# Optimization experiments

Measured on AMD Instinct MI355X. Metric: run time of the kernel, lower is better.

## Reference

```python
import jax, jax.numpy as jnp
import numpy as np

B, L, D, DI, N, R = 2, 2048, 1024, 2048, 16, 64


def setup_inputs() -> dict:
    key = jax.random.key(0)
    ks = jax.random.split(key, 10)
    g = lambda k, shape, s: (jax.random.normal(k, shape, dtype=jnp.float32) * s)
    return {
        "x": g(ks[0], (B, L, D), 1.0),
        "in_w": g(ks[1], (DI, D), 0.02),
        "in_b": jnp.zeros((DI,), jnp.float32),
        "conv_w": g(ks[2], (DI, 1, 3), 0.2),
        "conv_b": jnp.zeros((DI,), jnp.float32),
        "x_proj_w": g(ks[3], (R + N, DI), 0.02),
        "x_proj_b": jnp.zeros((R + N,), jnp.float32),
        "dt_w": g(ks[4], (DI, R), 0.02),
        "dt_b": jnp.zeros((DI,), jnp.float32),
        "A_log": g(ks[5], (DI, N), 1.0),
        "D_param": g(ks[6], (DI,), 1.0),
        "out_w": g(ks[7], (D, DI), 0.02),
        "out_b": jnp.zeros((D,), jnp.float32),
    }


def _forward(x, in_w, in_b, conv_w, conv_b, x_proj_w, x_proj_b,
             dt_w, dt_b, A_log, D_param, out_w, out_b):
    b, l, d = x.shape
    di = in_w.shape[0]
    # in_proj
    h = x @ in_w.T + in_b                               # [b, l, di]
    # depthwise conv1d, kernel 3, padding 1 (output length == l, so the
    # torch [:, :, :l] slice is a no-op)
    hc = jnp.transpose(h, (0, 2, 1))                    # [b, di, l]
    hc = jax.lax.conv_general_dilated(
        hc, conv_w, window_strides=(1,), padding=[(1, 1)],
        dimension_numbers=("NCH", "OIH", "NCH"), feature_group_count=di)
    hc = hc + conv_b[None, :, None]
    u = jax.nn.silu(jnp.transpose(hc, (0, 2, 1)))       # [b, l, di]
    # ssm (dropout is identity in eval mode)
    A = -jnp.exp(A_log)                                 # [di, n]
    x_dbl = u @ x_proj_w.T + x_proj_b                   # [b, l, r+n]
    r = dt_w.shape[1]
    delta_lr, Bm = x_dbl[..., :r], x_dbl[..., r:]       # [b,l,r], [b,l,n]
    delta = jax.nn.softplus(delta_lr @ dt_w.T + dt_b)   # [b, l, di]
    deltaA = jnp.exp(jnp.einsum("bld,dn->bldn", delta, A))        # [b,l,di,n]
    deltaBu = jnp.einsum("bld,bln->bldn", delta * u, Bm)          # [b,l,di,n]

    def step(carry, inp):
        dA, dBu = inp
        carry = dA * carry + dBu
        return carry, carry.sum(-1)

    init = jnp.zeros((b, di, A.shape[1]), dtype=deltaA.dtype)
    _, ys = jax.lax.scan(step, init,
                         (jnp.swapaxes(deltaA, 0, 1), jnp.swapaxes(deltaBu, 0, 1)))
    y = jnp.swapaxes(ys, 0, 1) + u * D_param            # [b, l, di]
    return y @ out_w.T + out_b                          # [b, l, d]


def reference(x, in_w, in_b, conv_w, conv_b, x_proj_w, x_proj_b,
              dt_w, dt_b, A_log, D_param, out_w, out_b):
    return _forward(x, in_w, in_b, conv_w, conv_b, x_proj_w, x_proj_b,
                    dt_w, dt_b, A_log, D_param, out_w, out_b)
```

## Files before the change

kernel.cpp:

```cpp
#include <hip/hip_runtime.h>

#define B_  2
#define L_  2048
#define D_  1024
#define DI_ 2048
#define NS  16
#define RR  64
#define MM  (B_*L_)
#define NC  32
#define CL  (L_/NC)
#define XKS 8

typedef __attribute__((ext_vector_type(8))) short bf16x8;
typedef __attribute__((ext_vector_type(4))) float f32x4;

__device__ __forceinline__ ushort f2bf_rn(float f) {
    union { float f; unsigned u; } v; v.f = f;
    unsigned r = v.u + 0x7FFF + ((v.u >> 16) & 1);
    return (ushort)(r >> 16);
}
__device__ __forceinline__ float bf2f(ushort h) {
    union { unsigned u; float f; } v; v.u = ((unsigned)h) << 16;
    return v.f;
}
__device__ __forceinline__ void gload_lds16(const ushort* g, ushort* l) {
    __builtin_amdgcn_global_load_lds(
        (const __attribute__((address_space(1))) void*)(g),
        (__attribute__((address_space(3))) void*)(l), 16, 0, 0);
}

__global__ __launch_bounds__(256)
void cvt_hilo(const float* __restrict__ in, ushort* __restrict__ hi,
              ushort* __restrict__ lo, int n4)
{
    int i = blockIdx.x * 256 + threadIdx.x;
    if (i >= n4) return;
    float4 v = ((const float4*)in)[i];
    ushort4 h, l;
    h.x = f2bf_rn(v.x); l.x = f2bf_rn(v.x - bf2f(h.x));
    h.y = f2bf_rn(v.y); l.y = f2bf_rn(v.y - bf2f(h.y));
    h.z = f2bf_rn(v.z); l.z = f2bf_rn(v.z - bf2f(h.z));
    h.w = f2bf_rn(v.w); l.w = f2bf_rn(v.w - bf2f(h.w));
    ((ushort4*)hi)[i] = h; ((ushort4*)lo)[i] = l;
}

__global__ __launch_bounds__(256, 2)
void gemm_bf16x3(const ushort* __restrict__ Ah, const ushort* __restrict__ Al,
                 const ushort* __restrict__ Bh, const ushort* __restrict__ Bl,
                 const float* __restrict__ bias, float* __restrict__ C,
                 int lda, int N, int kPerSplit)
{
    __shared__ ushort sAh[128*32], sAl[128*32], sBh[128*32], sBl[128*32];
    const int t    = threadIdx.x;
    const int bm   = blockIdx.y * 128, bn = blockIdx.x * 128;
    const int lane = t & 63, w = t >> 6;
    const int wr   = (w >> 1) * 64, wc = (w & 1) * 64;
    const int l16  = lane & 15;
    const int kbeg = blockIdx.z * kPerSplit;
    const int kend = kbeg + kPerSplit;
    C += (size_t)blockIdx.z * MM * N;

    const int srow  = lane >> 2;
    const int sslot = (lane & 3) ^ ((lane >> 3) & 3);
    const int r0 = 32 * w + srow, r1 = r0 + 16;
    const ushort* gAh0 = Ah + (size_t)(bm + r0) * lda + sslot * 8 + kbeg;
    const ushort* gAh1 = Ah + (size_t)(bm + r1) * lda + sslot * 8 + kbeg;
    const ushort* gAl0 = Al + (size_t)(bm + r0) * lda + sslot * 8 + kbeg;
    const ushort* gAl1 = Al + (size_t)(bm + r1) * lda + sslot * 8 + kbeg;
    const ushort* gBh0 = Bh + (size_t)(bn + r0) * lda + sslot * 8 + kbeg;
    const ushort* gBh1 = Bh + (size_t)(bn + r1) * lda + sslot * 8 + kbeg;
    const ushort* gBl0 = Bl + (size_t)(bn + r0) * lda + sslot * 8 + kbeg;
    const ushort* gBl1 = Bl + (size_t)(bn + r1) * lda + sslot * 8 + kbeg;
    ushort* lA0 = sAh + 1024 * w;
    ushort* lA1 = sAh + 1024 * w + 512;
    ushort* lAl0 = sAl + 1024 * w, *lAl1 = sAl + 1024 * w + 512;
    ushort* lB0 = sBh + 1024 * w, *lB1 = sBh + 1024 * w + 512;
    ushort* lBl0 = sBl + 1024 * w, *lBl1 = sBl + 1024 * w + 512;

    const int swz = ((lane >> 4) ^ ((l16 >> 1) & 3));
    const int offA = (wr + l16) * 32 + swz * 8;
    const int offB = (wc + l16) * 32 + swz * 8;

    f32x4 acc[4][4];
    #pragma unroll
    for (int i = 0; i < 4; ++i)
        #pragma unroll
        for (int j = 0; j < 4; ++j)
            acc[i][j] = (f32x4){0.f, 0.f, 0.f, 0.f};

    for (int k0 = 0; k0 < kPerSplit; k0 += 32) {
        gload_lds16(gAh0 + k0, lA0);  gload_lds16(gAh1 + k0, lA1);
        gload_lds16(gAl0 + k0, lAl0); gload_lds16(gAl1 + k0, lAl1);
        gload_lds16(gBh0 + k0, lB0);  gload_lds16(gBh1 + k0, lB1);
        gload_lds16(gBl0 + k0, lBl0); gload_lds16(gBl1 + k0, lBl1);
        __syncthreads();
        bf16x8 fbh[4], fbl[4];
        #pragma unroll
        for (int nj = 0; nj < 4; ++nj) {
            fbh[nj] = *(const bf16x8*)(sBh + offB + nj * 512);
            fbl[nj] = *(const bf16x8*)(sBl + offB + nj * 512);
        }
        #pragma unroll
        for (int mi = 0; mi < 4; ++mi) {
            bf16x8 fah = *(const bf16x8*)(sAh + offA + mi * 512);
            bf16x8 fal = *(const bf16x8*)(sAl + offA + mi * 512);
            #pragma unroll
            for (int nj = 0; nj < 4; ++nj) {
                acc[mi][nj] = __builtin_amdgcn_mfma_f32_16x16x32_bf16(fah, fbh[nj], acc[mi][nj], 0, 0, 0);
                acc[mi][nj] = __builtin_amdgcn_mfma_f32_16x16x32_bf16(fah, fbl[nj], acc[mi][nj], 0, 0, 0);
                acc[mi][nj] = __builtin_amdgcn_mfma_f32_16x16x32_bf16(fal, fbh[nj], acc[mi][nj], 0, 0, 0);
            }
        }
        __syncthreads();
    }
    #pragma unroll
    for (int nj = 0; nj < 4; ++nj) {
        int col = bn + wc + nj * 16 + l16;
        float bb = bias ? bias[col] : 0.f;
        #pragma unroll
        for (int mi = 0; mi < 4; ++mi) {
            int row0 = bm + wr + mi * 16 + (lane >> 4) * 4;
            #pragma unroll
            for (int r = 0; r < 4; ++r)
                C[(size_t)(row0 + r) * N + col] = acc[mi][nj][r] + bb;
        }
    }
}

__global__ __launch_bounds__(256)
void combine2(const float* __restrict__ part, const float* __restrict__ ob,
              float* __restrict__ out)
{
    int i = blockIdx.x * 256 + threadIdx.x;
    float4 a = ((const float4*)part)[i];
    float4 b = ((const float4*)(part + (size_t)MM * D_))[i];
    float4 bb = *(const float4*)(ob + ((i & (D_/4 - 1)) << 2));
    float4 o;
    o.x = a.x + b.x + bb.x; o.y = a.y + b.y + bb.y;
    o.z = a.z + b.z + bb.z; o.w = a.w + b.w + bb.w;
    ((float4*)out)[i] = o;
}

__global__ __launch_bounds__(256)
void conv_silu(const float* __restrict__ h, const float* __restrict__ cw,
               const float* __restrict__ cb, float* __restrict__ u)
{
    size_t idx = (size_t)blockIdx.x * 256 + threadIdx.x;
    int    di  = idx & (DI_ - 1);
    size_t bl  = idx >> 11;
    int    l   = (int)(bl & (L_ - 1));
    float s = cb[di] + h[idx] * cw[di * 3 + 1];
    if (l > 0)      s += h[idx - DI_] * cw[di * 3 + 0];
    if (l < L_ - 1) s += h[idx + DI_] * cw[di * 3 + 2];
    u[idx] = s / (1.f + __expf(-s));
}

__global__ __launch_bounds__(256)
void xprojA(const float* __restrict__ u, const float* __restrict__ xw,
            float* __restrict__ part)
{
    __shared__ float ut[32][132];
    __shared__ float wt[80][132];
    const int t  = threadIdx.x;
    const int bm = blockIdx.x * 32;
    const int ks = blockIdx.y;
    const int r2 = t & 15, cg = t >> 4;
    float acc[2][5] = {};
    for (int ch = 0; ch < 2; ++ch) {
        const int kb = ks * 256 + ch * 128;
        {
            int sr = t >> 3, k4 = (t & 7) * 4;
            #pragma unroll
            for (int i = 0; i < 4; ++i) {
                float4 v = *(const float4*)(u + (size_t)(bm + sr) * DI_ + kb + k4 + 32 * i);
                ut[sr][k4 + 32*i + 0] = v.x; ut[sr][k4 + 32*i + 1] = v.y;
                ut[sr][k4 + 32*i + 2] = v.z; ut[sr][k4 + 32*i + 3] = v.w;
            }
        }
        #pragma unroll
        for (int i = 0; i < 10; ++i) {
            int idx = t + 256 * i;
            int wrow = idx >> 5, k4 = (idx & 31) * 4;
            float4 v = *(const float4*)(xw + (size_t)wrow * DI_ + kb + k4);
            wt[wrow][k4 + 0] = v.x; wt[wrow][k4 + 1] = v.y;
            wt[wrow][k4 + 2] = v.z; wt[wrow][k4 + 3] = v.w;
        }
        __syncthreads();
        for (int k = 0; k < 128; k += 4) {
            float4 u0 = *(const float4*)&ut[r2][k];
            float4 u1 = *(const float4*)&ut[r2 + 16][k];
            #pragma unroll
            for (int c = 0; c < 5; ++c) {
                float4 wv = *(const float4*)&wt[cg * 5 + c][k];
                acc[0][c] = fmaf(u0.x, wv.x, fmaf(u0.y, wv.y, fmaf(u0.z, wv.z, fmaf(u0.w, wv.w, acc[0][c]))));
                acc[1][c] = fmaf(u1.x, wv.x, fmaf(u1.y, wv.y, fmaf(u1.z, wv.z, fmaf(u1.w, wv.w, acc[1][c]))));
            }
        }
        __syncthreads();
    }
    size_t b0 = ((size_t)ks * MM + bm + r2) * 80 + cg * 5;
    size_t b1 = ((size_t)ks * MM + bm + r2 + 16) * 80 + cg * 5;
    #pragma unroll
    for (int c = 0; c < 5; ++c) { part[b0 + c] = acc[0][c]; part[b1 + c] = acc[1][c]; }
}

__global__ __launch_bounds__(256)
void xprojB(const float* __restrict__ part, const float* __restrict__ xpb,
            float* __restrict__ xdbl)
{
    int idx = blockIdx.x * 256 + threadIdx.x;
    int c = idx % 80;
    float s = xpb[c];
    #pragma unroll
    for (int sl = 0; sl < XKS; ++sl)
        s += part[(size_t)sl * (MM * 80) + idx];
    xdbl[idx] = s;
}

__global__ __launch_bounds__(256)
void transpose_dtw(const float* __restrict__ dtw, float* __restrict__ dtwT)
{
    int idx = blockIdx.x * 256 + threadIdx.x;
    int di  = idx & (DI_ - 1);
    int r   = idx >> 11;
    dtwT[(size_t)r * DI_ + di] = dtw[(size_t)di * RR + r];
}

__global__ __launch_bounds__(256)
void delta_gemm(const float* __restrict__ xdbl, const float* __restrict__ dtwT,
                const float* __restrict__ dtb, float* __restrict__ delta)
{
    __shared__ float dl[16][64];
    const int t    = threadIdx.x;
    const int row0 = blockIdx.y * 16;
    const int col  = blockIdx.x * 256 + t;
    {
        int sr = t >> 4, sk = (t & 15) << 2;
        float4 v = *(const float4*)(xdbl + (size_t)(row0 + sr) * 80 + sk);
        dl[sr][sk] = v.x; dl[sr][sk+1] = v.y; dl[sr][sk+2] = v.z; dl[sr][sk+3] = v.w;
    }
    __syncthreads();
    float acc[16] = {};
    for (int k = 0; k < 64; ++k) {
        float w = dtwT[(size_t)k * DI_ + col];
        #pragma unroll
        for (int rr = 0; rr < 16; ++rr)
            acc[rr] = fmaf(dl[rr][k], w, acc[rr]);
    }
    float bias = dtb[col];
    #pragma unroll
    for (int rr = 0; rr < 16; ++rr) {
        float x  = acc[rr] + bias;
        float sp = fmaxf(x, 0.f) + log1pf(__expf(-fabsf(x)));
        delta[(size_t)(row0 + rr) * DI_ + col] = sp;
    }
}

__global__ __launch_bounds__(256)
void scanA(const float* __restrict__ delta, const float* __restrict__ u,
           const float* __restrict__ xdbl, const float* __restrict__ A_log,
           float* __restrict__ Pbuf, float* __restrict__ Sbuf)
{
    const int tid  = blockIdx.x * 256 + threadIdx.x;
    const int di   = tid & (DI_ - 1);
    const int rest = tid >> 11;
    const int ch   = rest & (NC - 1);
    const int b    = rest >> 5;
    float A2[NS];
    {
        const float4* ap = (const float4*)(A_log + (size_t)di * NS);
        #pragma unroll
        for (int q = 0; q < 4; ++q) {
            float4 v = ap[q];
            A2[q*4+0] = -__expf(v.x) * 1.44269504f;
            A2[q*4+1] = -__expf(v.y) * 1.44269504f;
            A2[q*4+2] = -__expf(v.z) * 1.44269504f;
            A2[q*4+3] = -__expf(v.w) * 1.44269504f;
        }
    }
    float c[NS], P[NS];
    #pragma unroll
    for (int n = 0; n < NS; ++n) { c[n] = 0.f; P[n] = 1.f; }
    const size_t l0 = (size_t)b * L_ + (size_t)ch * CL;
    const float* dp = delta + l0 * DI_ + di;
    const float* up = u     + l0 * DI_ + di;
    const float* xp = xdbl  + l0 * 80 + RR;
    for (int l = 0; l < CL; ++l) {
        float dlt = dp[(size_t)l * DI_];
        float du  = dlt * up[(size_t)l * DI_];
        const float4* bp = (const float4*)(xp + (size_t)l * 80);
        #pragma unroll
        for (int q = 0; q < 4; ++q) {
            float4 bv = bp[q];
            float bn_[4] = {bv.x, bv.y, bv.z, bv.w};
            #pragma unroll
            for (int j = 0; j < 4; ++j) {
                int   n = q * 4 + j;
                float a = exp2f(dlt * A2[n]);
                c[n] = fmaf(a, c[n], du * bn_[j]);
                P[n] *= a;
            }
        }
    }
    float4* Pp = (float4*)(Pbuf + (size_t)tid * NS);
    float4* Sp = (float4*)(Sbuf + (size_t)tid * NS);
    #pragma unroll
    for (int q = 0; q < 4; ++q) {
        Pp[q] = make_float4(P[q*4], P[q*4+1], P[q*4+2], P[q*4+3]);
        Sp[q] = make_float4(c[q*4], c[q*4+1], c[q*4+2], c[q*4+3]);
    }
}

__global__ __launch_bounds__(256)
void scanB(const float* __restrict__ Pbuf, const float* __restrict__ Sbuf,
           float* __restrict__ start)
{
    const int tid = blockIdx.x * 256 + threadIdx.x;
    const int n   = tid & (NS - 1);
    const int di  = (tid >> 4) & (DI_ - 1);
    const int b   = tid >> 15;
    float c = 0.f;
    for (int ch = 0; ch < NC; ++ch) {
        size_t idx = ((size_t)(b * NC + ch) * DI_ + di) * NS + n;
        start[idx] = c;
        c = fmaf(Pbuf[idx], c, Sbuf[idx]);
    }
}

__global__ __launch_bounds__(256)
void scanC(const float* __restrict__ delta, const float* __restrict__ u,
           const float* __restrict__ xdbl, const float* __restrict__ A_log,
           const float* __restrict__ Dp, const float* __restrict__ start,
           ushort* __restrict__ yh, ushort* __restrict__ yl)
{
    const int tid  = blockIdx.x * 256 + threadIdx.x;
    const int di   = tid & (DI_ - 1);
    const int rest = tid >> 11;
    const int ch   = rest & (NC - 1);
    const int b    = rest >> 5;
    float A2[NS];
    {
        const float4* ap = (const float4*)(A_log + (size_t)di * NS);
        #pragma unroll
        for (int q = 0; q < 4; ++q) {
            float4 v = ap[q];
            A2[q*4+0] = -__expf(v.x) * 1.44269504f;
            A2[q*4+1] = -__expf(v.y) * 1.44269504f;
            A2[q*4+2] = -__expf(v.z) * 1.44269504f;
            A2[q*4+3] = -__expf(v.w) * 1.44269504f;
        }
    }
    float c[NS];
    {
        const float4* sp = (const float4*)(start + (size_t)tid * NS);
        #pragma unroll
        for (int q = 0; q < 4; ++q) {
            float4 v = sp[q];
            c[q*4+0] = v.x; c[q*4+1] = v.y; c[q*4+2] = v.z; c[q*4+3] = v.w;
        }
    }
    const float Dpar = Dp[di];
    const size_t l0 = (size_t)b * L_ + (size_t)ch * CL;
    const float* dp = delta + l0 * DI_ + di;
    const float* up = u     + l0 * DI_ + di;
    const float* xp = xdbl  + l0 * 80 + RR;
    for (int l = 0; l < CL; ++l) {
        float dlt = dp[(size_t)l * DI_];
        float uu  = up[(size_t)l * DI_];
        float du  = dlt * uu;
        const float4* bp = (const float4*)(xp + (size_t)l * 80);
        float sum = 0.f;
        #pragma unroll
        for (int q = 0; q < 4; ++q) {
            float4 bv = bp[q];
            float bn_[4] = {bv.x, bv.y, bv.z, bv.w};
            #pragma unroll
            for (int j = 0; j < 4; ++j) {
                int   n = q * 4 + j;
                float a = exp2f(dlt * A2[n]);
                c[n] = fmaf(a, c[n], du * bn_[j]);
                sum += c[n];
            }
        }
        float y = sum + uu * Dpar;
        ushort hb = f2bf_rn(y);
        size_t oi = (l0 + l) * DI_ + di;
        yh[oi] = hb;
        yl[oi] = f2bf_rn(y - bf2f(hb));
    }
}

extern "C" void kernel_launch(void* const* d_in, const int* in_sizes, int n_in,
                              void* d_out, int out_size, void* d_ws, size_t ws_size,
                              hipStream_t stream)
{
    const float* x      = (const float*)d_in[0];
    const float* in_w   = (const float*)d_in[1];
    const float* in_b   = (const float*)d_in[2];
    const float* conv_w = (const float*)d_in[3];
    const float* conv_b = (const float*)d_in[4];
    const float* xpw    = (const float*)d_in[5];
    const float* xpb    = (const float*)d_in[6];
    const float* dt_w   = (const float*)d_in[7];
    const float* dt_b   = (const float*)d_in[8];
    const float* A_log  = (const float*)d_in[9];
    const float* Dpar   = (const float*)d_in[10];
    const float* out_w  = (const float*)d_in[11];
    const float* out_b  = (const float*)d_in[12];
    float*       out    = (float*)d_out;

    char* ws  = (char*)d_ws;
    size_t off = 0;
    auto alloc = [&](size_t bytes) {
        void* p = ws + off; off = (off + bytes + 255) & ~(size_t)255; return p;
    };
    const size_t pse = (size_t)B_ * NC * DI_ * NS;
    float*  u_    = (float*)alloc((size_t)MM * DI_ * 4);
    float*  h_    = (float*)alloc((size_t)MM * DI_ * 4);
    float*  xdbl  = (float*)alloc((size_t)MM * 80 * 4);
    float*  dtwT  = (float*)alloc((size_t)RR * DI_ * 4);
    ushort* yh    = (ushort*)alloc((size_t)MM * DI_ * 2);
    ushort* yl    = (ushort*)alloc((size_t)MM * DI_ * 2);
    float*  stbuf = (float*)alloc(pse * 4);
    ushort* xh    = (ushort*)alloc((size_t)MM * D_ * 2);
    ushort* xl    = (ushort*)alloc((size_t)MM * D_ * 2);
    ushort* wih   = (ushort*)alloc((size_t)DI_ * D_ * 2);
    ushort* wil   = (ushort*)alloc((size_t)DI_ * D_ * 2);
    ushort* woh   = (ushort*)alloc((size_t)D_ * DI_ * 2);
    ushort* wol   = (ushort*)alloc((size_t)D_ * DI_ * 2);
    float*  xpart = (float*)yh;
    float*  Pbuf  = (float*)yh;
    float*  Sbuf  = (float*)yl;
    float*  part2 = u_;

    cvt_hilo<<<(MM * D_ / 4 + 255) / 256, 256, 0, stream>>>(x, xh, xl, MM * D_ / 4);
    cvt_hilo<<<(DI_ * D_ / 4 + 255) / 256, 256, 0, stream>>>(in_w, wih, wil, DI_ * D_ / 4);
    cvt_hilo<<<(D_ * DI_ / 4 + 255) / 256, 256, 0, stream>>>(out_w, woh, wol, D_ * DI_ / 4);
    gemm_bf16x3<<<dim3(DI_ / 128, MM / 128, 1), 256, 0, stream>>>(
        xh, xl, wih, wil, in_b, h_, D_, DI_, D_);
    conv_silu<<<(MM * DI_) / 256, 256, 0, stream>>>(h_, conv_w, conv_b, u_);
    xprojA<<<dim3(MM / 32, XKS), 256, 0, stream>>>(u_, xpw, xpart);
    xprojB<<<(MM * 80) / 256, 256, 0, stream>>>(xpart, xpb, xdbl);
    transpose_dtw<<<(RR * DI_) / 256, 256, 0, stream>>>(dt_w, dtwT);
    delta_gemm<<<dim3(DI_ / 256, MM / 16), 256, 0, stream>>>(xdbl, dtwT, dt_b, h_);
    scanA<<<(B_ * NC * DI_) / 256, 256, 0, stream>>>(h_, u_, xdbl, A_log, Pbuf, Sbuf);
    scanB<<<(B_ * DI_ * NS) / 256, 256, 0, stream>>>(Pbuf, Sbuf, stbuf);
    scanC<<<(B_ * NC * DI_) / 256, 256, 0, stream>>>(h_, u_, xdbl, A_log, Dpar, stbuf, yh, yl);
    gemm_bf16x3<<<dim3(D_ / 128, MM / 128, 2), 256, 0, stream>>>(
        yh, yl, woh, wol, nullptr, part2, DI_, D_, DI_ / 2);
    combine2<<<(MM * D_ / 4) / 256, 256, 0, stream>>>(part2, out_b, out);
}
```

Baseline: 454.4 us.

## Double scan chunk count and vectorize conv_silu with float4 accesses

Raises the number of scan chunks per sequence from 32 to 64, doubling the thread count in the two chunked-scan passes and halving each chunk's serial length. The chunk-state buffer now aliases the bf16 input-split buffer to save workspace. conv_silu also switches to float4 loads and stores, with four channels per thread. The cost is longer serial carry chains and more partial-state traffic in scanB, and the buffer aliasing must fit inside the xh allocation.

```diff
diff --git a/kernel.cpp b/kernel.cpp
--- a/kernel.cpp
+++ b/kernel.cpp
@@ -7,7 +7,7 @@
 #define NS  16
 #define RR  64
 #define MM  (B_*L_)
-#define NC  32
+#define NC  64
 #define CL  (L_/NC)
 #define XKS 8
 
@@ -57,7 +57,6 @@
     const int wr   = (w >> 1) * 64, wc = (w & 1) * 64;
     const int l16  = lane & 15;
     const int kbeg = blockIdx.z * kPerSplit;
-    const int kend = kbeg + kPerSplit;
     C += (size_t)blockIdx.z * MM * N;
 
     const int srow  = lane >> 2;
@@ -145,14 +144,27 @@
 void conv_silu(const float* __restrict__ h, const float* __restrict__ cw,
                const float* __restrict__ cb, float* __restrict__ u)
 {
-    size_t idx = (size_t)blockIdx.x * 256 + threadIdx.x;
-    int    di  = idx & (DI_ - 1);
-    size_t bl  = idx >> 11;
-    int    l   = (int)(bl & (L_ - 1));
-    float s = cb[di] + h[idx] * cw[di * 3 + 1];
-    if (l > 0)      s += h[idx - DI_] * cw[di * 3 + 0];
-    if (l < L_ - 1) s += h[idx + DI_] * cw[di * 3 + 2];
-    u[idx] = s / (1.f + __expf(-s));
+    size_t i4 = ((size_t)blockIdx.x * 256 + threadIdx.x) << 2;
+    int    di = (int)(i4 & (DI_ - 1));
+    int    l  = (int)((i4 >> 11) & (L_ - 1));
+    float4 cc = *(const float4*)(h + i4);
+    float4 lf = make_float4(0.f, 0.f, 0.f, 0.f);
+    float4 rt = make_float4(0.f, 0.f, 0.f, 0.f);
+    if (l > 0)      lf = *(const float4*)(h + i4 - DI_);
+    if (l < L_ - 1) rt = *(const float4*)(h + i4 + DI_);
+    float4 bb = *(const float4*)(cb + di);
+    float cin[4]  = {cc.x, cc.y, cc.z, cc.w};
+    float lin[4]  = {lf.x, lf.y, lf.z, lf.w};
+    float rin[4]  = {rt.x, rt.y, rt.z, rt.w};
+    float bin[4]  = {bb.x, bb.y, bb.z, bb.w};
+    float res[4];
+    #pragma unroll
+    for (int j = 0; j < 4; ++j) {
+        const float* w = cw + (size_t)(di + j) * 3;
+        float s = bin[j] + lin[j] * w[0] + cin[j] * w[1] + rin[j] * w[2];
+        res[j] = s / (1.f + __expf(-s));
+    }
+    *(float4*)(u + i4) = make_float4(res[0], res[1], res[2], res[3]);
 }
 
 __global__ __launch_bounds__(256)
@@ -265,7 +277,7 @@
     const int di   = tid & (DI_ - 1);
     const int rest = tid >> 11;
     const int ch   = rest & (NC - 1);
-    const int b    = rest >> 5;
+    const int b    = rest >> 6;
     float A2[NS];
     {
         const float4* ap = (const float4*)(A_log + (size_t)di * NS);
@@ -337,7 +349,7 @@
     const int di   = tid & (DI_ - 1);
     const int rest = tid >> 11;
     const int ch   = rest & (NC - 1);
-    const int b    = rest >> 5;
+    const int b    = rest >> 6;
     float A2[NS];
     {
         const float4* ap = (const float4*)(A_log + (size_t)di * NS);
@@ -414,14 +426,12 @@
     auto alloc = [&](size_t bytes) {
         void* p = ws + off; off = (off + bytes + 255) & ~(size_t)255; return p;
     };
-    const size_t pse = (size_t)B_ * NC * DI_ * NS;
     float*  u_    = (float*)alloc((size_t)MM * DI_ * 4);
     float*  h_    = (float*)alloc((size_t)MM * DI_ * 4);
     float*  xdbl  = (float*)alloc((size_t)MM * 80 * 4);
     float*  dtwT  = (float*)alloc((size_t)RR * DI_ * 4);
     ushort* yh    = (ushort*)alloc((size_t)MM * DI_ * 2);
     ushort* yl    = (ushort*)alloc((size_t)MM * DI_ * 2);
-    float*  stbuf = (float*)alloc(pse * 4);
     ushort* xh    = (ushort*)alloc((size_t)MM * D_ * 2);
     ushort* xl    = (ushort*)alloc((size_t)MM * D_ * 2);
     ushort* wih   = (ushort*)alloc((size_t)DI_ * D_ * 2);
@@ -431,6 +441,7 @@
     float*  xpart = (float*)yh;
     float*  Pbuf  = (float*)yh;
     float*  Sbuf  = (float*)yl;
+    float*  stbuf = (float*)xh;
     float*  part2 = u_;
 
     cvt_hilo<<<(MM * D_ / 4 + 255) / 256, 256, 0, stream>>>(x, xh, xl, MM * D_ / 4);
@@ -438,7 +449,7 @@
     cvt_hilo<<<(D_ * DI_ / 4 + 255) / 256, 256, 0, stream>>>(out_w, woh, wol, D_ * DI_ / 4);
     gemm_bf16x3<<<dim3(DI_ / 128, MM / 128, 1), 256, 0, stream>>>(
         xh, xl, wih, wil, in_b, h_, D_, DI_, D_);
-    conv_silu<<<(MM * DI_) / 256, 256, 0, stream>>>(h_, conv_w, conv_b, u_);
+    conv_silu<<<(MM * DI_ / 4) / 256, 256, 0, stream>>>(h_, conv_w, conv_b, u_);
     xprojA<<<dim3(MM / 32, XKS), 256, 0, stream>>>(u_, xpw, xpart);
     xprojB<<<(MM * 80) / 256, 256, 0, stream>>>(xpart, xpb, xdbl);
     transpose_dtw<<<(RR * DI_) / 256, 256, 0, stream>>>(dt_w, dtwT);
```

After: 434.4 us. 4.4% less time.
